# Performance work log

Hardware: AMD Instinct MI355X
Metric: run time of the kernel (lower is better)

The kernel has to match this reference:

```python
import jax, jax.numpy as jnp
import numpy as np

B, L, XS, YS, A, C, NL = 32, 4096, 256, 256, 4, 64, 5  # batch, seq, x_size, y_size, n_actions, hid_cnn, cnn_layers


def _conv2d(x, w):
    # x: [N,Cin,H,W], w: [Cout,Cin,3,3], stride 1, pad 1 ('SAME')
    return jax.lax.conv_general_dilated(x, w, (1, 1), 'SAME',
                                        dimension_numbers=('NCHW', 'OIHW', 'NCHW'))


def setup_inputs() -> dict:
    key = jax.random.key(0)
    ks = jax.random.split(key, 16)
    stdv = 1.0 / np.sqrt(XS)
    inp = {
        'x': jax.random.normal(ks[0], (B, L, XS), jnp.float32),
        'y': jax.random.normal(ks[1], (B, YS), jnp.float32),
        'x_mask': jax.random.randint(ks[2], (B, L), 0, 2) == 1,
        'actions': jax.random.randint(ks[3], (B,), 0, A),
        'weight': jax.random.uniform(ks[4], (YS, XS), jnp.float32, -stdv, stdv),
    }
    chans = [(1, C)] + [(C, C)] * (NL - 2) + [(C, 1)]
    for i, (ci, co) in enumerate(chans):
        bound = 1.0 / np.sqrt(ci * 9)
        inp[f'cw{i}'] = jax.random.uniform(ks[5 + 2 * i], (A, co, ci, 3, 3), jnp.float32, -bound, bound)
        inp[f'cb{i}'] = jax.random.uniform(ks[6 + 2 * i], (A, co), jnp.float32, -bound, bound)
    return inp


def reference(x, y, x_mask, actions, weight,
              cw0, cb0, cw1, cb1, cw2, cb2, cw3, cb3, cw4, cb4):
    img = weight[None, None]  # [1,1,YS,XS] -- weight matrix as a 1-channel image

    def per_action(w0, b0, w1, b1, w2, b2, w3, b3, w4, b4):
        out = img
        layers = ((w0, b0), (w1, b1), (w2, b2), (w3, b3), (w4, b4))
        for i, (w, b) in enumerate(layers):
            out = _conv2d(out, w) + b[None, :, None, None]
            if i < NL - 1:
                out = jax.nn.relu(out)
        return out[0, 0]  # [YS,XS]

    # all per-action conv stacks batched via vmap -> [A,YS,XS]
    W_a = jax.vmap(per_action)(cw0, cb0, cw1, cb1, cw2, cb2, cw3, cb3, cw4, cb4)
    # one-hot multiply + sum over actions == select the per-sample action matrix
    Wy = jnp.einsum('bh,bhx->bx', y, W_a[actions])          # [B,XS]
    xWy = jnp.einsum('blx,bx->bl', x, Wy)                   # [B,L]
    xWy = jnp.where(x_mask, -jnp.inf, xWy)
    return jax.nn.softmax(xWy, axis=-1)  # eval-mode output (training uses log_softmax)
```

## Files before the change

kernel.cpp:

```cpp
#include <hip/hip_runtime.h>
#include <cstdint>
#include <cstddef>

typedef __attribute__((ext_vector_type(8))) short bf16x8;
typedef __attribute__((ext_vector_type(4))) float f32x4;
typedef __attribute__((ext_vector_type(4))) int i32x4;

__device__ inline unsigned short cvt_bf16_rne(float f) {
    unsigned u = __builtin_bit_cast(unsigned, f);
    u = (u + 0x7FFFu + ((u >> 16) & 1u)) >> 16;
    return (unsigned short)u;
}
__device__ inline float bf16_to_f32(unsigned short s) {
    return __builtin_bit_cast(float, (unsigned)s << 16);
}

__global__ void detect_mask_kernel(const unsigned int* m, int* flag) {
    int i = blockIdx.x * blockDim.x + threadIdx.x;
    int f = 0;
    #pragma unroll
    for (int k = 0; k < 4; ++k) {
        unsigned int v = m[i * 4 + k];
        if (v == 0x3F800000u) f |= 2;
        else if (v > 1u) f |= 1;
    }
    if (f) atomicOr(flag, f);
}

__global__ void apack_all_kernel(const float* __restrict__ cw1,
                                 const float* __restrict__ cw2,
                                 const float* __restrict__ cw3,
                                 char* __restrict__ apack,
                                 int* __restrict__ flag) {
    int t = threadIdx.x;
    int tap = blockIdx.x, a = blockIdx.y, lz = blockIdx.z;
    if (tap == 0 && a == 0 && lz == 0 && t == 0) *flag = 0;
    const float* cw = (lz == 0) ? cw1 : (lz == 1 ? cw2 : cw3);
    char* outp = apack + (size_t)lz * 294912;
    int ks = t >> 8, mf = (t >> 6) & 3, lane = t & 63;
    int n = lane & 15, q = lane >> 4;
    int co = mf * 16 + n;
    int ci0 = ks * 32 + q * 8;
    unsigned d[4];
    #pragma unroll
    for (int jj = 0; jj < 4; ++jj) {
        unsigned short h0 = cvt_bf16_rne(cw[((size_t)(a * 64 + co) * 64 + ci0 + 2 * jj + 0) * 9 + tap]);
        unsigned short h1 = cvt_bf16_rne(cw[((size_t)(a * 64 + co) * 64 + ci0 + 2 * jj + 1) * 9 + tap]);
        d[jj] = (unsigned)h0 | ((unsigned)h1 << 16);
    }
    *(i32x4*)(outp + ((((size_t)(a * 9 + tap) * 2 + ks) * 4 + mf) * 1024 + lane * 16)) =
        *(i32x4*)d;
}

__device__ __forceinline__ void conv_mid_body(const i32x4* lds4,
                                              const char* __restrict__ apack_l,
                                              const float* __restrict__ cb,
                                              unsigned short* __restrict__ act_out,
                                              int a, int r0, int c0, int tid) {
    int lane = tid & 63, wv = tid >> 6;
    int n = lane & 15, q = lane >> 4;

    f32x4 acc[4][4];
    #pragma unroll
    for (int mf = 0; mf < 4; ++mf) {
        f32x4 bb = *(const f32x4*)(cb + a * 64 + mf * 16 + q * 4);
        #pragma unroll
        for (int nf = 0; nf < 4; ++nf) acc[mf][nf] = bb;
    }

    int base_nf[4];
    #pragma unroll
    for (int nf = 0; nf < 4; ++nf) {
        int orl = wv * 2 + (nf >> 1);
        int ocl = ((nf & 1) << 4) + n;
        base_nf[nf] = (orl * 34 + ocl) * 9 + q;
    }
    const char* ap = apack_l + (size_t)a * 9 * 8192 + lane * 16;

    #pragma unroll
    for (int tap = 0; tap < 9; ++tap) {
        const int ty = tap / 3, tx = tap - ty * 3;
        const int toff = (ty * 34 + tx) * 9;
        #pragma unroll
        for (int ks = 0; ks < 2; ++ks) {
            bf16x8 Af[4], Bf[4];
            #pragma unroll
            for (int mf = 0; mf < 4; ++mf)
                Af[mf] = __builtin_bit_cast(bf16x8,
                    *(const i32x4*)(ap + (((tap * 2 + ks) * 4 + mf) << 10)));
            #pragma unroll
            for (int nf = 0; nf < 4; ++nf)
                Bf[nf] = __builtin_bit_cast(bf16x8, lds4[base_nf[nf] + toff + ks * 4]);
            #pragma unroll
            for (int mf = 0; mf < 4; ++mf)
                #pragma unroll
                for (int nf = 0; nf < 4; ++nf)
                    acc[mf][nf] = __builtin_amdgcn_mfma_f32_16x16x32_bf16(
                        Af[mf], Bf[nf], acc[mf][nf], 0, 0, 0);
        }
    }

    #pragma unroll
    for (int nf = 0; nf < 4; ++nf) {
        int grow = r0 + wv * 2 + (nf >> 1);
        int gcol = c0 + ((nf & 1) << 4) + n;
        char* ob = (char*)act_out + (((size_t)(a << 16) + (grow << 8) + gcol) << 7) + q * 8;
        #pragma unroll
        for (int mf = 0; mf < 4; ++mf) {
            f32x4 v = acc[mf][nf];
            unsigned d0 = (unsigned)cvt_bf16_rne(fmaxf(v.x, 0.0f))
                        | ((unsigned)cvt_bf16_rne(fmaxf(v.y, 0.0f)) << 16);
            unsigned d1 = (unsigned)cvt_bf16_rne(fmaxf(v.z, 0.0f))
                        | ((unsigned)cvt_bf16_rne(fmaxf(v.w, 0.0f)) << 16);
            uint2 st; st.x = d0; st.y = d1;
            *(uint2*)(ob + mf * 32) = st;
        }
    }
}

__global__ __launch_bounds__(256, 3)
void conv_mid_mfma(const unsigned short* __restrict__ act_in,
                   const char* __restrict__ apack_l,
                   const float* __restrict__ cb,
                   unsigned short* __restrict__ act_out) {
    __shared__ i32x4 lds4[340 * 9];
    int tid = threadIdx.x;
    int a = blockIdx.z;
    int r0 = blockIdx.y * 8, c0 = blockIdx.x * 32;
    const char* actb = (const char*)act_in;

    for (int s = tid; s < 2720; s += 256) {
        int px = s >> 3, o = s & 7;
        int prow = px / 34, pcol = px - prow * 34;
        int grow = r0 - 1 + prow, gcol = c0 - 1 + pcol;
        i32x4 v = {0, 0, 0, 0};
        if ((unsigned)grow < 256u && (unsigned)gcol < 256u)
            v = *(const i32x4*)(actb + (((size_t)(a << 16) + (grow << 8) + gcol) << 7) + (o << 4));
        lds4[px * 9 + o] = v;
    }
    __syncthreads();
    conv_mid_body(lds4, apack_l, cb, act_out, a, r0, c0, tid);
}

__global__ __launch_bounds__(256, 3)
void conv_mid_fused0(const float* __restrict__ img,
                     const float* __restrict__ cw0,
                     const float* __restrict__ cb0,
                     const char* __restrict__ apack_l,
                     const float* __restrict__ cb,
                     unsigned short* __restrict__ act_out) {
    __shared__ i32x4 lds4[340 * 9];
    __shared__ float img_s[12 * 36];
    int tid = threadIdx.x;
    int a = blockIdx.z;
    int r0 = blockIdx.y * 8, c0 = blockIdx.x * 32;

    for (int s = tid; s < 432; s += 256) {
        int ir = s / 36, ic = s - ir * 36;
        int gr = r0 - 2 + ir, gc = c0 - 2 + ic;
        img_s[s] = ((unsigned)gr < 256u && (unsigned)gc < 256u) ? img[gr * 256 + gc] : 0.0f;
    }
    __syncthreads();

    int o = tid & 7;
    float wr[8][9], br[8];
    #pragma unroll
    for (int j = 0; j < 8; ++j) {
        const float* wp = cw0 + ((size_t)a * 64 + o * 8 + j) * 9;
        #pragma unroll
        for (int t = 0; t < 9; ++t) wr[j][t] = wp[t];
        br[j] = cb0[a * 64 + o * 8 + j];
    }

    for (int s = tid; s < 2720; s += 256) {
        int px = s >> 3;
        int prow = px / 34, pcol = px - prow * 34;
        int grow = r0 - 1 + prow, gcol = c0 - 1 + pcol;
        i32x4 v = {0, 0, 0, 0};
        if ((unsigned)grow < 256u && (unsigned)gcol < 256u) {
            float accv[8];
            #pragma unroll
            for (int j = 0; j < 8; ++j) accv[j] = br[j];
            #pragma unroll
            for (int dy = 0; dy < 3; ++dy)
                #pragma unroll
                for (int dx = 0; dx < 3; ++dx) {
                    float iv = img_s[(prow + dy) * 36 + (pcol + dx)];
                    #pragma unroll
                    for (int j = 0; j < 8; ++j)
                        accv[j] = fmaf(wr[j][dy * 3 + dx], iv, accv[j]);
                }
            unsigned d[4];
            #pragma unroll
            for (int jj = 0; jj < 4; ++jj) {
                unsigned short h0 = cvt_bf16_rne(fmaxf(accv[2 * jj + 0], 0.0f));
                unsigned short h1 = cvt_bf16_rne(fmaxf(accv[2 * jj + 1], 0.0f));
                d[jj] = (unsigned)h0 | ((unsigned)h1 << 16);
            }
            v = *(i32x4*)d;
        }
        lds4[px * 9 + o] = v;
    }
    __syncthreads();
    conv_mid_body(lds4, apack_l, cb, act_out, a, r0, c0, tid);
}

__global__ void conv_last_kernel(const unsigned short* __restrict__ act,
                                 const float* __restrict__ cw4,
                                 const float* __restrict__ cb4,
                                 float* __restrict__ W_a) {
    int y = blockIdx.x, a = blockIdx.y;
    int tid = threadIdx.x;
    int lane = tid & 63, wv = tid >> 6;
    int o = lane & 7, pl = lane >> 3;
    float wr[8][9];
    #pragma unroll
    for (int j = 0; j < 8; ++j) {
        const float* wp = cw4 + ((size_t)a * 64 + o * 8 + j) * 9;
        #pragma unroll
        for (int t = 0; t < 9; ++t) wr[j][t] = wp[t];
    }
    const char* actb = (const char*)act;
    float bias = cb4[a];
    for (int i = 0; i < 8; ++i) {
        int x = i * 32 + wv * 8 + pl;
        float p = 0.0f;
        #pragma unroll
        for (int ty = 0; ty < 3; ++ty) {
            int py = y + ty - 1;
            #pragma unroll
            for (int tx = 0; tx < 3; ++tx) {
                int px = x + tx - 1;
                if ((unsigned)py < 256u && (unsigned)px < 256u) {
                    i32x4 v = *(const i32x4*)(actb +
                        (((size_t)(a << 16) + (py << 8) + px) << 7) + (o << 4));
                    const unsigned* dv = (const unsigned*)&v;
                    #pragma unroll
                    for (int j = 0; j < 8; ++j) {
                        unsigned d = dv[j >> 1];
                        unsigned short us = (j & 1) ? (unsigned short)(d >> 16)
                                                    : (unsigned short)(d & 0xffffu);
                        p = fmaf(bf16_to_f32(us), wr[j][ty * 3 + tx], p);
                    }
                }
            }
        }
        p += __shfl_xor(p, 1, 64);
        p += __shfl_xor(p, 2, 64);
        p += __shfl_xor(p, 4, 64);
        if (o == 0) W_a[(size_t)(a << 16) + (y << 8) + x] = p + bias;
    }
}

__global__ void wy_kernel(const float* __restrict__ yv,
                          const int* __restrict__ actions,
                          const float* __restrict__ W_a,
                          float* __restrict__ Wy) {
    int b = blockIdx.x, t = threadIdx.x;
    int x = t >> 2, hq = t & 3;
    int a = actions[b];
    const float* Wp = W_a + (size_t)a * 65536;
    const float* yb = yv + b * 256;
    float acc = 0.0f;
    #pragma unroll 8
    for (int i = 0; i < 64; ++i) {
        int h = i * 4 + hq;
        acc = fmaf(yb[h], Wp[(size_t)h * 256 + x], acc);
    }
    acc += __shfl_xor(acc, 1, 64);
    acc += __shfl_xor(acc, 2, 64);
    if (hq == 0) Wy[b * 256 + x] = acc;
}

__global__ void logits_kernel(const float* __restrict__ xv,
                              const void* __restrict__ mask,
                              const int* __restrict__ flag,
                              const float* __restrict__ Wy,
                              float* __restrict__ out) {
    __shared__ float part[4][64][36];
    int tid = threadIdx.x, lane = tid & 63, w = tid >> 6;
    int b = blockIdx.y;
    int fl = *flag;
    float4 wy4 = *(const float4*)(Wy + b * 256 + lane * 4);
    const float* xb = xv + (size_t)b * 4096 * 256;
    int slot = (lane & 15) | ((lane >> 5) << 4);
    bool wr = (lane & 16) == 0;
    float ninf = -__builtin_inff();

    #pragma unroll
    for (int pass = 0; pass < 2; ++pass) {
        int rowbase = blockIdx.x * 512 + pass * 256 + w * 64;
        #pragma unroll 4
        for (int li = 0; li < 64; ++li) {
            const float4 x4 = *(const float4*)(xb + (size_t)(rowbase + li) * 256 + lane * 4);
            float p = x4.x * wy4.x + x4.y * wy4.y + x4.z * wy4.z + x4.w * wy4.w;
            p += __shfl_xor(p, 16, 64);
            if (wr) part[w][li][slot] = p;
        }
        float s = 0.0f;
        #pragma unroll
        for (int j = 0; j < 8; ++j) {
            f32x4 v4 = *(const f32x4*)&part[w][lane][j * 4];
            s += (v4.x + v4.y) + (v4.z + v4.w);
        }
        int r = rowbase + lane;
        size_t mi = (size_t)b * 4096 + r;
        bool msk;
        if (fl & 2)      msk = ((const float*)mask)[mi] != 0.0f;
        else if (fl & 1) msk = ((const unsigned char*)mask)[mi] != 0;
        else             msk = ((const int*)mask)[mi] != 0;
        out[mi] = msk ? ninf : s;
        __syncthreads();
    }
}

__global__ void softmax_kernel(float* __restrict__ out) {
    int b = blockIdx.x, tid = threadIdx.x;
    int lane = tid & 63, wid = tid >> 6;
    float* row = out + (size_t)b * 4096;
    float v[4];
    float m = -__builtin_inff();
    #pragma unroll
    for (int i = 0; i < 4; ++i) { v[i] = row[tid + i * 1024]; m = fmaxf(m, v[i]); }
    #pragma unroll
    for (int off = 32; off > 0; off >>= 1) m = fmaxf(m, __shfl_xor(m, off, 64));
    __shared__ float redm[16];
    __shared__ float reds[16];
    if (lane == 0) redm[wid] = m;
    __syncthreads();
    float M = redm[0];
    #pragma unroll
    for (int j = 1; j < 16; ++j) M = fmaxf(M, redm[j]);
    float s = 0.0f;
    #pragma unroll
    for (int i = 0; i < 4; ++i) { v[i] = expf(v[i] - M); s += v[i]; }
    #pragma unroll
    for (int off = 32; off > 0; off >>= 1) s += __shfl_xor(s, off, 64);
    if (lane == 0) reds[wid] = s;
    __syncthreads();
    float S = 0.0f;
    #pragma unroll
    for (int j = 0; j < 16; ++j) S += reds[j];
    float inv = 1.0f / S;
    #pragma unroll
    for (int i = 0; i < 4; ++i) row[tid + i * 1024] = v[i] * inv;
}

extern "C" void kernel_launch(void* const* d_in, const int* in_sizes, int n_in,
                              void* d_out, int out_size, void* d_ws, size_t ws_size,
                              hipStream_t stream) {
    const float* xv      = (const float*)d_in[0];
    const float* yv      = (const float*)d_in[1];
    const void*  xmask   = d_in[2];
    const int*   actions = (const int*)d_in[3];
    const float* weight  = (const float*)d_in[4];
    const float* cw0 = (const float*)d_in[5];
    const float* cb0 = (const float*)d_in[6];
    const float* cw1 = (const float*)d_in[7];
    const float* cb1 = (const float*)d_in[8];
    const float* cw2 = (const float*)d_in[9];
    const float* cb2 = (const float*)d_in[10];
    const float* cw3 = (const float*)d_in[11];
    const float* cb3 = (const float*)d_in[12];
    const float* cw4 = (const float*)d_in[13];
    const float* cb4 = (const float*)d_in[14];
    float* out = (float*)d_out;

    char* ws = (char*)d_ws;
    unsigned short* bufA = (unsigned short*)ws;
    unsigned short* bufB = (unsigned short*)(ws + 33554432);
    char*  apack = ws + 67108864;
    float* W_a   = (float*)(ws + 67993600);
    float* Wy    = (float*)(ws + 69042176);
    int*   flag  = (int*)(ws + 69074944);

    apack_all_kernel<<<dim3(9, 4, 3), 512, 0, stream>>>(cw1, cw2, cw3, apack, flag);
    detect_mask_kernel<<<32, 256, 0, stream>>>((const unsigned int*)xmask, flag);

    conv_mid_fused0<<<dim3(8, 32, 4), 256, 0, stream>>>(weight, cw0, cb0, apack, cb1, bufA);
    conv_mid_mfma<<<dim3(8, 32, 4), 256, 0, stream>>>(bufA, apack + 294912, cb2, bufB);
    conv_mid_mfma<<<dim3(8, 32, 4), 256, 0, stream>>>(bufB, apack + 589824, cb3, bufA);
    conv_last_kernel<<<dim3(256, 4), 256, 0, stream>>>(bufA, cw4, cb4, W_a);

    wy_kernel<<<32, 1024, 0, stream>>>(yv, actions, W_a, Wy);
    logits_kernel<<<dim3(8, 32), 256, 0, stream>>>(xv, xmask, flag, Wy, out);
    softmax_kernel<<<32, 1024, 0, stream>>>(out);
}
```

Measured before the change: 401.4 us.

## Restructure logits kernel to one wave per row group with shuffle reduction

Rewrites the x·Wy logits kernel so each wave computes 8 rows at a time with full-wave shuffle reductions instead of an LDS partial-sum table. The grid grows from 8 to 64 blocks per batch, so more loads are in flight across the GPU. This drops shared memory and __syncthreads but adds many more cross-lane shuffles and serial lane-0 mask reads and stores.

```diff
diff --git a/kernel.cpp b/kernel.cpp
--- a/kernel.cpp
+++ b/kernel.cpp
@@ -272,45 +272,57 @@
     if (hq == 0) Wy[b * 256 + x] = acc;
 }
 
-__global__ void logits_kernel(const float* __restrict__ xv,
-                              const void* __restrict__ mask,
-                              const int* __restrict__ flag,
-                              const float* __restrict__ Wy,
-                              float* __restrict__ out) {
-    __shared__ float part[4][64][36];
+__global__ __launch_bounds__(256)
+void logits_kernel(const float* __restrict__ xv,
+                   const void* __restrict__ mask,
+                   const int* __restrict__ flag,
+                   const float* __restrict__ Wy,
+                   float* __restrict__ out) {
     int tid = threadIdx.x, lane = tid & 63, w = tid >> 6;
     int b = blockIdx.y;
     int fl = *flag;
     float4 wy4 = *(const float4*)(Wy + b * 256 + lane * 4);
     const float* xb = xv + (size_t)b * 4096 * 256;
-    int slot = (lane & 15) | ((lane >> 5) << 4);
-    bool wr = (lane & 16) == 0;
     float ninf = -__builtin_inff();
-
-    #pragma unroll
-    for (int pass = 0; pass < 2; ++pass) {
-        int rowbase = blockIdx.x * 512 + pass * 256 + w * 64;
-        #pragma unroll 4
-        for (int li = 0; li < 64; ++li) {
-            const float4 x4 = *(const float4*)(xb + (size_t)(rowbase + li) * 256 + lane * 4);
-            float p = x4.x * wy4.x + x4.y * wy4.y + x4.z * wy4.z + x4.w * wy4.w;
-            p += __shfl_xor(p, 16, 64);
-            if (wr) part[w][li][slot] = p;
-        }
-        float s = 0.0f;
+    int base0 = blockIdx.x * 64 + w * 16;
+
+    #pragma unroll
+    for (int it = 0; it < 2; ++it) {
+        int base = base0 + it * 8;
+        size_t mi = (size_t)b * 4096 + base;
+        bool m[8];
+        if (lane == 0) {
+            if (fl & 2) {
+                const float* mp = (const float*)mask + mi;
+                #pragma unroll
+                for (int j = 0; j < 8; ++j) m[j] = mp[j] != 0.0f;
+            } else if (fl & 1) {
+                const unsigned char* mp = (const unsigned char*)mask + mi;
+                #pragma unroll
+                for (int j = 0; j < 8; ++j) m[j] = mp[j] != 0;
+            } else {
+                const int* mp = (const int*)mask + mi;
+                #pragma unroll
+                for (int j = 0; j < 8; ++j) m[j] = mp[j] != 0;
+            }
+        }
+        const float* rp = xb + (size_t)base * 256 + lane * 4;
+        float p[8];
         #pragma unroll
         for (int j = 0; j < 8; ++j) {
-            f32x4 v4 = *(const f32x4*)&part[w][lane][j * 4];
-            s += (v4.x + v4.y) + (v4.z + v4.w);
-        }
-        int r = rowbase + lane;
-        size_t mi = (size_t)b * 4096 + r;
-        bool msk;
-        if (fl & 2)      msk = ((const float*)mask)[mi] != 0.0f;
-        else if (fl & 1) msk = ((const unsigned char*)mask)[mi] != 0;
-        else             msk = ((const int*)mask)[mi] != 0;
-        out[mi] = msk ? ninf : s;
-        __syncthreads();
+            float4 x4 = *(const float4*)(rp + j * 256);
+            p[j] = x4.x * wy4.x + x4.y * wy4.y + x4.z * wy4.z + x4.w * wy4.w;
+        }
+        #pragma unroll
+        for (int off = 32; off > 0; off >>= 1)
+            #pragma unroll
+            for (int j = 0; j < 8; ++j)
+                p[j] += __shfl_xor(p[j], off, 64);
+        if (lane == 0) {
+            #pragma unroll
+            for (int j = 0; j < 8; ++j)
+                out[mi + j] = m[j] ? ninf : p[j];
+        }
     }
 }
 
@@ -383,6 +395,6 @@
     conv_last_kernel<<<dim3(256, 4), 256, 0, stream>>>(bufA, cw4, cb4, W_a);
 
     wy_kernel<<<32, 1024, 0, stream>>>(yv, actions, W_a, Wy);
-    logits_kernel<<<dim3(8, 32), 256, 0, stream>>>(xv, xmask, flag, Wy, out);
+    logits_kernel<<<dim3(64, 32), 256, 0, stream>>>(xv, xmask, flag, Wy, out);
     softmax_kernel<<<32, 1024, 0, stream>>>(out);
 }
```

After: 360.2 us. 1.11x faster.

## Restructure logits kernel: 16 lanes per row, shuffle reduction, 8x more blocks

Applied to the files above, without the earlier changes.

Rewrites the x·Wy logits kernel so each group of 16 lanes handles one row, with each lane loading four float4 chunks, followed by a shuffle-tree reduction. This removes the shared-memory partial buffer and the barriers. The grid grows from 8x32 to 64x32 blocks so more memory requests are in flight across CUs for this bandwidth-bound 128MB read. The trade-off is that each block does less work, and each row's mask is read and its result written by a single lane.

```diff
diff --git a/kernel.cpp b/kernel.cpp
--- a/kernel.cpp
+++ b/kernel.cpp
@@ -272,45 +272,52 @@
     if (hq == 0) Wy[b * 256 + x] = acc;
 }
 
-__global__ void logits_kernel(const float* __restrict__ xv,
-                              const void* __restrict__ mask,
-                              const int* __restrict__ flag,
-                              const float* __restrict__ Wy,
-                              float* __restrict__ out) {
-    __shared__ float part[4][64][36];
+__global__ __launch_bounds__(256)
+void logits_kernel(const float* __restrict__ xv,
+                   const void* __restrict__ mask,
+                   const int* __restrict__ flag,
+                   const float* __restrict__ Wy,
+                   float* __restrict__ out) {
     int tid = threadIdx.x, lane = tid & 63, w = tid >> 6;
+    int i = lane & 15, r = lane >> 4;
     int b = blockIdx.y;
     int fl = *flag;
-    float4 wy4 = *(const float4*)(Wy + b * 256 + lane * 4);
+    float4 wyv[4];
+    #pragma unroll
+    for (int k = 0; k < 4; ++k)
+        wyv[k] = *(const float4*)(Wy + b * 256 + k * 64 + i * 4);
     const float* xb = xv + (size_t)b * 4096 * 256;
-    int slot = (lane & 15) | ((lane >> 5) << 4);
-    bool wr = (lane & 16) == 0;
     float ninf = -__builtin_inff();
-
-    #pragma unroll
-    for (int pass = 0; pass < 2; ++pass) {
-        int rowbase = blockIdx.x * 512 + pass * 256 + w * 64;
-        #pragma unroll 4
-        for (int li = 0; li < 64; ++li) {
-            const float4 x4 = *(const float4*)(xb + (size_t)(rowbase + li) * 256 + lane * 4);
-            float p = x4.x * wy4.x + x4.y * wy4.y + x4.z * wy4.z + x4.w * wy4.w;
-            p += __shfl_xor(p, 16, 64);
-            if (wr) part[w][li][slot] = p;
-        }
-        float s = 0.0f;
-        #pragma unroll
-        for (int j = 0; j < 8; ++j) {
-            f32x4 v4 = *(const f32x4*)&part[w][lane][j * 4];
-            s += (v4.x + v4.y) + (v4.z + v4.w);
-        }
-        int r = rowbase + lane;
-        size_t mi = (size_t)b * 4096 + r;
-        bool msk;
-        if (fl & 2)      msk = ((const float*)mask)[mi] != 0.0f;
-        else if (fl & 1) msk = ((const unsigned char*)mask)[mi] != 0;
-        else             msk = ((const int*)mask)[mi] != 0;
-        out[mi] = msk ? ninf : s;
-        __syncthreads();
+    int base0 = blockIdx.x * 64 + w * 16;
+
+    #pragma unroll 1
+    for (int it = 0; it < 4; ++it) {
+        int row = base0 + it * 4 + r;
+        const float* rp = xb + (size_t)row * 256 + i * 4;
+        float4 xq[4];
+        #pragma unroll
+        for (int k = 0; k < 4; ++k)
+            xq[k] = *(const float4*)(rp + k * 64);
+        float p = 0.0f;
+        #pragma unroll
+        for (int k = 0; k < 4; ++k) {
+            p = fmaf(xq[k].x, wyv[k].x, p);
+            p = fmaf(xq[k].y, wyv[k].y, p);
+            p = fmaf(xq[k].z, wyv[k].z, p);
+            p = fmaf(xq[k].w, wyv[k].w, p);
+        }
+        p += __shfl_xor(p, 8, 64);
+        p += __shfl_xor(p, 4, 64);
+        p += __shfl_xor(p, 2, 64);
+        p += __shfl_xor(p, 1, 64);
+        if (i == 0) {
+            size_t mi = (size_t)b * 4096 + row;
+            bool msk;
+            if (fl & 2)      msk = ((const float*)mask)[mi] != 0.0f;
+            else if (fl & 1) msk = ((const unsigned char*)mask)[mi] != 0;
+            else             msk = ((const int*)mask)[mi] != 0;
+            out[mi] = msk ? ninf : p;
+        }
     }
 }
 
@@ -383,6 +390,6 @@
     conv_last_kernel<<<dim3(256, 4), 256, 0, stream>>>(bufA, cw4, cb4, W_a);
 
     wy_kernel<<<32, 1024, 0, stream>>>(yv, actions, W_a, Wy);
-    logits_kernel<<<dim3(8, 32), 256, 0, stream>>>(xv, xmask, flag, Wy, out);
+    logits_kernel<<<dim3(64, 32), 256, 0, stream>>>(xv, xmask, flag, Wy, out);
     softmax_kernel<<<32, 1024, 0, stream>>>(out);
 }
```

Result: faster. 358.4 us (-10.7%).
